# Optimization experiments

Hardware: AMD Instinct MI355X
Metric: run time of the kernel (lower is better)

## Reference

```python
import jax, jax.numpy as jnp
import numpy as np

G, B, K, D = 16384, 4, 2, 64
NEG = -1e30


def _mlp3(x, w1, b1, w2, b2, w3, b3):
    # MLP: linear->relu x3 (BatchNorm defined but unused in original forward)
    h = jax.nn.relu(x @ w1 + b1)
    h = jax.nn.relu(h @ w2 + b2)
    return jax.nn.relu(h @ w3 + b3)


def setup_inputs() -> dict:
    key = jax.random.key(0)
    ks = jax.random.split(key, 32)

    def lin(k, fan_in, fan_out):
        k1, k2 = jax.random.split(k)
        s = 1.0 / np.sqrt(fan_in)
        w = jax.random.uniform(k1, (fan_in, fan_out), jnp.float32, -s, s)
        b = jax.random.uniform(k2, (fan_out,), jnp.float32, -s, s)
        return w, b

    inp = {}
    inp['ap_feat'] = jax.random.normal(ks[0], (G, B, 1), jnp.float32)
    inp['e_feat'] = jax.random.normal(ks[1], (G, B, K, 2), jnp.float32)
    inp['w_pre_ap'], inp['b_pre_ap'] = lin(ks[2], 1, D)
    inp['w_pre_edge'], inp['b_pre_edge'] = lin(ks[3], 2, D)
    # mlp_update_5 (AP-side neighbor messages), _6 (UE-side), _7 (edge update)
    inp['w5_1'], inp['b5_1'] = lin(ks[4], 2 * D, D)
    inp['w5_2'], inp['b5_2'] = lin(ks[5], D, D)
    inp['w5_3'], inp['b5_3'] = lin(ks[6], D, D)
    inp['w6_1'], inp['b6_1'] = lin(ks[7], 2 * D, D)
    inp['w6_2'], inp['b6_2'] = lin(ks[8], D, D)
    inp['w6_3'], inp['b6_3'] = lin(ks[9], D, D)
    inp['w7_1'], inp['b7_1'] = lin(ks[10], 2 * D, D)
    inp['w7_2'], inp['b7_2'] = lin(ks[11], D, D)
    inp['w7_3'], inp['b7_3'] = lin(ks[12], D, D)
    inp['w_post'], inp['b_post'] = lin(ks[13], D, 2)
    return inp


def _edge_conv(e, a, w5_1, b5_1, w5_2, b5_2, w5_3, b5_3,
               w6_1, b6_1, w6_2, b6_2, w6_3, b6_3,
               w7_1, b7_1, w7_2, b7_2, w7_3, b7_3):
    # e: [G,B,K,D] AP2UE edge hid; a: [G,B,D] AP hid.
    # M1[g,b,j] = mlp5(cat(a[g,b], e[g,b,j])) -- same-AP neighbor edges
    x1 = jnp.concatenate([jnp.broadcast_to(a[:, :, None, :], e.shape), e], axis=-1)  # [G,B,K,2D]
    M1 = _mlp3(x1, w5_1, b5_1, w5_2, b5_2, w5_3, b5_3)  # [G,B,K,D]
    # M2[g,b,bp,k] = mlp6(cat(a[g,b], e[g,bp,k])) -- same-UE neighbor edges
    # (original uses the SRC AP feature here too). Split first linear to
    # avoid materializing the [G,B,B,K,2D] concat.
    h = jax.nn.relu(
        (a @ w6_1[:D])[:, :, None, None, :]
        + (e @ w6_1[D:])[:, None, :, :, :]
        + b6_1)  # [G,B,B,K,D]
    h = jax.nn.relu(h @ w6_2 + b6_2)
    M2 = jax.nn.relu(h @ w6_3 + b6_3)  # [G,B,Bp,K,D]
    # masked max excluding the edge itself
    eyeK = jnp.eye(K, dtype=bool)  # [k, j]
    m1max = jnp.max(jnp.where(eyeK[None, None, :, :, None], NEG,
                              M1[:, :, None, :, :]), axis=3)  # [G,B,K,D]
    eyeB = jnp.eye(B, dtype=bool)  # [b, bp]
    m2max = jnp.max(jnp.where(eyeB[None, :, :, None, None], NEG, M2), axis=2)  # [G,B,K,D]
    agg = jnp.maximum(m1max, m2max)
    # new edge feature: mlp7(cat(agg, e_hid))
    return _mlp3(jnp.concatenate([agg, e], axis=-1),
                 w7_1, b7_1, w7_2, b7_2, w7_3, b7_3)


def reference(ap_feat, e_feat, w_pre_ap, b_pre_ap, w_pre_edge, b_pre_edge,
              w5_1, b5_1, w5_2, b5_2, w5_3, b5_3,
              w6_1, b6_1, w6_2, b6_2, w6_3, b6_3,
              w7_1, b7_1, w7_2, b7_2, w7_3, b7_3,
              w_post, b_post):
    # PreLayer (live branches only: AP nodes and AP2UE edges; APConv/UEConv
    # write node 'new' which is never read, so UE/UE2AP branches are dead).
    a = jax.nn.relu(ap_feat @ w_pre_ap + b_pre_ap)   # [G,B,D]
    e = jax.nn.relu(e_feat @ w_pre_edge + b_pre_edge)  # [G,B,K,D]
    # two UpdateLayers (shared weights: ModuleList([UpdateLayer()]*2) + global MLPs)
    for _ in range(2):
        e = _edge_conv(e, a, w5_1, b5_1, w5_2, b5_2, w5_3, b5_3,
                       w6_1, b6_1, w6_2, b6_2, w6_3, b6_3,
                       w7_1, b7_1, w7_2, b7_2, w7_3, b7_3)
    out = e @ w_post + b_post  # [G,B,K,2]
    r, im = out[..., 0], out[..., 1]
    # norm_func: per-graph [B,K] complex matrix, each row (over K) L2-normalized
    n = jnp.sqrt(jnp.sum(r * r + im * im, axis=-1, keepdims=True))
    return jnp.stack([r / n, im / n], axis=-1)  # [G,B,K,2]
```

## Files before the change

### kernel.cpp

```cpp
#include <hip/hip_runtime.h>


typedef unsigned short u16;
typedef unsigned int   u32;
typedef __attribute__((ext_vector_type(8))) short short8_t;
typedef __attribute__((ext_vector_type(2))) short short2v;
typedef __attribute__((ext_vector_type(4))) float floatx4;

#define OFF_W51 0
#define OFF_W61 8192
#define OFF_W71 16384
#define OFF_W52 24576
#define OFF_W53 28672
#define OFF_W62 32768
#define OFF_W63 36864
#define OFF_W72 40960
#define OFF_W73 45056
#define WS_U16  49152

#define CB51 0
#define CB52 64
#define CB53 128
#define CB61 192
#define CB62 256
#define CB63 320
#define CB71 384
#define CB72 448
#define CB73 512
#define CWPO 576
#define CBPO 704
#define CWPA 768
#define CBPA 832
#define CWPE 896
#define CBPE 1024
#define CSZ  1088

#define PW_U16 1536

struct Params {
  const float *ap, *ef;
  const float *wpa, *bpa, *wpe, *bpe;
  const float *w51, *b51, *w52, *b52, *w53, *b53;
  const float *w61, *b61, *w62, *b62, *w63, *b63;
  const float *w71, *b71, *w72, *b72, *w73, *b73;
  const float *wpost, *bpost;
  float *out;
  int gtot;
};

__device__ __forceinline__ u32 pk2(float a, float b) {
  const u32 ua = __float_as_uint(a) + 0x8000u;
  const u32 ub = __float_as_uint(b) + 0x8000u;
  return __builtin_amdgcn_perm(ub, ua, 0x07060302u);
}
__device__ __forceinline__ float blo(u32 v) { return __uint_as_float(v << 16); }
__device__ __forceinline__ float bhi(u32 v) { return __uint_as_float(v & 0xffff0000u); }
__device__ __forceinline__ u32 pkmax(u32 a, u32 b) {
  const short2v r = __builtin_elementwise_max(__builtin_bit_cast(short2v, a),
                                              __builtin_bit_cast(short2v, b));
  return __builtin_bit_cast(u32, r);
}
__device__ __forceinline__ u32 ror16(u32 x) { return (x >> 16) | (x << 16); }
__device__ __forceinline__ float sel4(int i, float x0, float x1, float x2, float x3) {
  const float lo = (i & 1) ? x1 : x0;
  const float hi = (i & 1) ? x3 : x2;
  return (i & 2) ? hi : lo;
}

__device__ __forceinline__ floatx4 mfma16(short8_t a, short8_t b, floatx4 c) {
  return __builtin_amdgcn_mfma_f32_16x16x32_bf16(a, b, c, 0, 0, 0);
}
__device__ __forceinline__ short8_t ldA(const u16* buf, int l) {
  return *(const short8_t*)(buf + l * 8);
}

template<int TSTRIDE>
__device__ __forceinline__ void layerK64R(floatx4* acc, short8_t a0, short8_t a1,
                                          const u16* B, int l) {
#pragma unroll
  for (int t = 0; t < 4; ++t) {
    const short8_t b0 = *(const short8_t*)(B + (t * TSTRIDE + 0) * 512 + l * 8);
    const short8_t b1 = *(const short8_t*)(B + (t * TSTRIDE + 1) * 512 + l * 8);
    acc[t] = mfma16(a0, b0, acc[t]);
    acc[t] = mfma16(a1, b1, acc[t]);
  }
}

__device__ __forceinline__ void layerK128R(floatx4* acc, short8_t a0, short8_t a1,
                                           short8_t a2, short8_t a3,
                                           const u16* B, int l) {
  short8_t a[4] = {a0, a1, a2, a3};
#pragma unroll
  for (int t = 0; t < 4; ++t)
#pragma unroll
    for (int h = 0; h < 4; ++h)
      acc[t] = mfma16(a[h], *(const short8_t*)(B + (t * 4 + h) * 512 + l * 8), acc[t]);
}

__device__ __forceinline__ void scatter_relu_bf16(u16* dst, const floatx4* acc, int q, int n) {
#pragma unroll
  for (int t = 0; t < 4; ++t) {
    const int kk = (t & 1) * 2 + (n >> 3);
    u16* base = dst + (t >> 1) * 512 + (n & 7);
    const u32 v01 = pk2(fmaxf(acc[t][0], 0.f), fmaxf(acc[t][1], 0.f));
    const u32 v23 = pk2(fmaxf(acc[t][2], 0.f), fmaxf(acc[t][3], 0.f));
    base[(4 * q + 0 + 16 * kk) * 8] = (u16)v01;
    base[(4 * q + 1 + 16 * kk) * 8] = (u16)(v01 >> 16);
    base[(4 * q + 2 + 16 * kk) * 8] = (u16)v23;
    base[(4 * q + 3 + 16 * kk) * 8] = (u16)(v23 >> 16);
  }
}

__device__ __forceinline__ void scatter_bf16(u16* dst, const floatx4* acc, int q, int n) {
#pragma unroll
  for (int t = 0; t < 4; ++t) {
    const int kk = (t & 1) * 2 + (n >> 3);
    u16* base = dst + (t >> 1) * 512 + (n & 7);
    const u32 v01 = pk2(acc[t][0], acc[t][1]);
    const u32 v23 = pk2(acc[t][2], acc[t][3]);
    base[(4 * q + 0 + 16 * kk) * 8] = (u16)v01;
    base[(4 * q + 1 + 16 * kk) * 8] = (u16)(v01 >> 16);
    base[(4 * q + 2 + 16 * kk) * 8] = (u16)v23;
    base[(4 * q + 3 + 16 * kk) * 8] = (u16)(v23 >> 16);
  }
}

__device__ __forceinline__ void scatter_pk(u16* dst, const u32* src, int q, int n) {
#pragma unroll
  for (int t = 0; t < 4; ++t) {
    const int kk = (t & 1) * 2 + (n >> 3);
    u16* base = dst + (t >> 1) * 512 + (n & 7);
#pragma unroll
    for (int half = 0; half < 2; ++half) {
      const u32 v = src[2 * t + half];
      base[(4 * q + 2 * half + 0 + 16 * kk) * 8] = (u16)v;
      base[(4 * q + 2 * half + 1 + 16 * kk) * 8] = (u16)(v >> 16);
    }
  }
}

__device__ __forceinline__ void scatter_aP(u16* dst, const floatx4* acc, int q, int n,
                                           const float* cb61) {
#pragma unroll
  for (int t = 0; t < 4; ++t) {
    const int kk = (t & 1) * 2 + (n >> 3);
    u16* base = dst + (t >> 1) * 256 + (n & 7);
    const float bv = cb61[16 * t + n];
    const u32 v = pk2(acc[t][0] + bv, acc[t][2] + bv);
    base[(2 * q + 0 + 8 * kk) * 8] = (u16)v;
    base[(2 * q + 1 + 8 * kk) * 8] = (u16)(v >> 16);
  }
}

__device__ __forceinline__ void init_accL(floatx4* acc, const float* cb, int n) {
#pragma unroll
  for (int t = 0; t < 4; ++t) {
    const float b = cb[16 * t + n];
    floatx4 v; v[0] = b; v[1] = b; v[2] = b; v[3] = b;
    acc[t] = v;
  }
}

struct frag2 { short8_t f0, f1; };

__device__ __forceinline__ frag2 make_a(float apv, int q, const float* sc) {
  frag2 r;
#pragma unroll
  for (int h = 0; h < 2; ++h) {
    const int fb = 32 * h + 8 * q;
    const float4 wa0 = *(const float4*)(sc + CWPA + fb);
    const float4 wa1 = *(const float4*)(sc + CWPA + fb + 4);
    const float4 ba0 = *(const float4*)(sc + CBPA + fb);
    const float4 ba1 = *(const float4*)(sc + CBPA + fb + 4);
    uint4 pa;
    pa.x = pk2(fmaxf(fmaf(apv, wa0.x, ba0.x), 0.f), fmaxf(fmaf(apv, wa0.y, ba0.y), 0.f));
    pa.y = pk2(fmaxf(fmaf(apv, wa0.z, ba0.z), 0.f), fmaxf(fmaf(apv, wa0.w, ba0.w), 0.f));
    pa.z = pk2(fmaxf(fmaf(apv, wa1.x, ba1.x), 0.f), fmaxf(fmaf(apv, wa1.y, ba1.y), 0.f));
    pa.w = pk2(fmaxf(fmaf(apv, wa1.z, ba1.z), 0.f), fmaxf(fmaf(apv, wa1.w, ba1.w), 0.f));
    if (h == 0) r.f0 = __builtin_bit_cast(short8_t, pa);
    else        r.f1 = __builtin_bit_cast(short8_t, pa);
  }
  return r;
}

#define NBLK 256
#define NWAVE 16
#define PPW  2

__global__ __attribute__((amdgpu_waves_per_eu(4, 4), amdgpu_num_vgpr(128)))
__launch_bounds__(1024, 4)
void hetgnn_mfma(Params p) {
  __shared__ __align__(16) u16   sW[WS_U16];
  __shared__ __align__(16) u16   sAct[NWAVE * PW_U16];
  __shared__ __align__(16) float sConst[CSZ];

  const int tid  = threadIdx.x;
  const int wave = tid >> 6;
  const int l    = tid & 63;
  const int q    = l >> 4;
  const int n    = l & 15;

  {
    const float* mats[9] = {p.w51, p.w61, p.w71, p.w52, p.w53, p.w62, p.w63, p.w72, p.w73};
    for (int fi = wave; fi < 96; fi += NWAVE) {
      const float* W;
      int t, h;
      if (fi < 48) { W = mats[fi >> 4]; const int loc = fi & 15; t = loc >> 2; h = loc & 3; }
      else { const int j = fi - 48; W = mats[3 + (j >> 3)]; const int loc = j & 7; t = loc >> 1; h = loc & 1; }
      const int nn = 16 * t + n;
      const int k0 = 32 * h + q * 8;
      float w[8];
#pragma unroll
      for (int j = 0; j < 8; ++j) w[j] = W[(k0 + j) * 64 + nn];
      uint4 o;
      o.x = pk2(w[0], w[1]); o.y = pk2(w[2], w[3]);
      o.z = pk2(w[4], w[5]); o.w = pk2(w[6], w[7]);
      *(uint4*)(sW + fi * 512 + l * 8) = o;
    }
  }
  if (tid < 64) {
    sConst[CB51 + tid] = p.b51[tid];
    sConst[CB52 + tid] = p.b52[tid];
    sConst[CB53 + tid] = p.b53[tid];
    sConst[CB61 + tid] = p.b61[tid];
    sConst[CB62 + tid] = p.b62[tid];
    sConst[CB63 + tid] = p.b63[tid];
    sConst[CB71 + tid] = p.b71[tid];
    sConst[CB72 + tid] = p.b72[tid];
    sConst[CB73 + tid] = p.b73[tid];
    sConst[CWPA + tid] = p.wpa[tid];
    sConst[CBPA + tid] = p.bpa[tid];
    sConst[CBPE + tid] = p.bpe[tid];
  }
  if (tid < 128) {
    sConst[CWPO + tid] = p.wpost[tid];
    sConst[CWPE + tid] = p.wpe[tid];
  }
  if (tid < 2) sConst[CBPO + tid] = p.bpost[tid];
  __syncthreads();

  u16* BUF = sAct + wave * PW_U16;
  u16* aPb = BUF + 1024;

  const int wslot = blockIdx.x * NWAVE + wave;

  for (int pi = 0; pi < PPW; ++pi) {
    const int g0 = (wslot * PPW + pi) * 2;
    if (g0 + 2 > p.gtot) break;

    const float apv = p.ap[(g0 + (n >> 3)) * 4 + ((n >> 1) & 3)];
    const frag2 A = make_a(apv, q, sConst);
    short8_t e0, e1;
    {
      const float f0 = p.ef[(g0 + (n >> 3)) * 16 + (n & 7) * 2];
      const float f1 = p.ef[(g0 + (n >> 3)) * 16 + (n & 7) * 2 + 1];
#pragma unroll
      for (int h = 0; h < 2; ++h) {
        const int fb = 32 * h + 8 * q;
        const float4 w00 = *(const float4*)(sConst + CWPE + fb);
        const float4 w01 = *(const float4*)(sConst + CWPE + fb + 4);
        const float4 w10 = *(const float4*)(sConst + CWPE + 64 + fb);
        const float4 w11 = *(const float4*)(sConst + CWPE + 64 + fb + 4);
        const float4 be0 = *(const float4*)(sConst + CBPE + fb);
        const float4 be1 = *(const float4*)(sConst + CBPE + fb + 4);
        uint4 pe;
        pe.x = pk2(fmaxf(fmaf(f0, w00.x, fmaf(f1, w10.x, be0.x)), 0.f),
                   fmaxf(fmaf(f0, w00.y, fmaf(f1, w10.y, be0.y)), 0.f));
        pe.y = pk2(fmaxf(fmaf(f0, w00.z, fmaf(f1, w10.z, be0.z)), 0.f),
                   fmaxf(fmaf(f0, w00.w, fmaf(f1, w10.w, be0.w)), 0.f));
        pe.z = pk2(fmaxf(fmaf(f0, w01.x, fmaf(f1, w11.x, be1.x)), 0.f),
                   fmaxf(fmaf(f0, w01.y, fmaf(f1, w11.y, be1.y)), 0.f));
        pe.w = pk2(fmaxf(fmaf(f0, w01.z, fmaf(f1, w11.z, be1.z)), 0.f),
                   fmaxf(fmaf(f0, w01.w, fmaf(f1, w11.w, be1.w)), 0.f));
        if (h == 0) e0 = __builtin_bit_cast(short8_t, pe);
        else        e1 = __builtin_bit_cast(short8_t, pe);
      }
    }

    {
      floatx4 accA[4];
#pragma unroll
      for (int t = 0; t < 4; ++t) { accA[t][0] = 0.f; accA[t][1] = 0.f; accA[t][2] = 0.f; accA[t][3] = 0.f; }
      layerK64R<4>(accA, A.f0, A.f1, sW + OFF_W61, l);
      scatter_aP(aPb, accA, q, n, sConst + CB61);
    }

#pragma unroll 1
    for (int it = 0; it < 2; ++it) {
      if (it == 1) { e0 = ldA(BUF, l); e1 = ldA(BUF + 512, l); }

      u32 m1p[8];
      {
        floatx4 acc[4]; init_accL(acc, sConst + CB51, n);
        layerK128R(acc, A.f0, A.f1, e0, e1, sW + OFF_W51, l);
        scatter_relu_bf16(BUF, acc, q, n);
        floatx4 acc2[4]; init_accL(acc2, sConst + CB52, n);
        layerK64R<2>(acc2, ldA(BUF, l), ldA(BUF + 512, l), sW + OFF_W52, l);
        scatter_relu_bf16(BUF, acc2, q, n);
        floatx4 acc3[4]; init_accL(acc3, sConst + CB53, n);
        layerK64R<2>(acc3, ldA(BUF, l), ldA(BUF + 512, l), sW + OFF_W53, l);
#pragma unroll
        for (int t = 0; t < 4; ++t) {
          m1p[2 * t + 0] = pk2(acc3[t][0], acc3[t][1]);
          m1p[2 * t + 1] = pk2(acc3[t][2], acc3[t][3]);
        }
      }

      u32 m2p[8];
      {
        floatx4 accE[4];
#pragma unroll
        for (int t = 0; t < 4; ++t) { accE[t][0] = 0.f; accE[t][1] = 0.f; accE[t][2] = 0.f; accE[t][3] = 0.f; }
        layerK64R<4>(accE, e0, e1, sW + OFF_W61 + 2 * 512, l);
        scatter_bf16(BUF, accE, q, n);

        const int d = n >> 1;
        const int b_ln = d & 3;
        short8_t hf0[3], hf1[3];
#pragma unroll
        for (int j = 0; j < 3; ++j) {
          const int bp = (j >= b_ln) ? (j + 1) : j;
          const int re = (n & 8) + bp * 2 + (n & 1);
#pragma unroll
          for (int h = 0; h < 2; ++h) {
            const uint4 av = *(const uint4*)(aPb + h * 256 + (d + 8 * q) * 8);
            const uint4 ev = *(const uint4*)(BUF + h * 512 + (re + 16 * q) * 8);
            uint4 ph;
            ph.x = pk2(fmaxf(blo(av.x) + blo(ev.x), 0.f),
                       fmaxf(bhi(av.x) + bhi(ev.x), 0.f));
            ph.y = pk2(fmaxf(blo(av.y) + blo(ev.y), 0.f),
                       fmaxf(bhi(av.y) + bhi(ev.y), 0.f));
            ph.z = pk2(fmaxf(blo(av.z) + blo(ev.z), 0.f),
                       fmaxf(bhi(av.z) + bhi(ev.z), 0.f));
            ph.w = pk2(fmaxf(blo(av.w) + blo(ev.w), 0.f),
                       fmaxf(bhi(av.w) + bhi(ev.w), 0.f));
            if (h == 0) hf0[j] = __builtin_bit_cast(short8_t, ph);
            else        hf1[j] = __builtin_bit_cast(short8_t, ph);
          }
        }
#pragma unroll
        for (int j = 0; j < 3; ++j) {
          floatx4 acc2[4]; init_accL(acc2, sConst + CB62, n);
          layerK64R<2>(acc2, hf0[j], hf1[j], sW + OFF_W62, l);
          scatter_relu_bf16(BUF, acc2, q, n);
          floatx4 acc3[4]; init_accL(acc3, sConst + CB63, n);
          layerK64R<2>(acc3, ldA(BUF, l), ldA(BUF + 512, l), sW + OFF_W63, l);
#pragma unroll
          for (int t = 0; t < 4; ++t) {
#pragma unroll
            for (int h = 0; h < 2; ++h) {
              const u32 cand = pk2(acc3[t][2 * h], acc3[t][2 * h + 1]);
              m2p[2 * t + h] = (j == 0) ? cand : pkmax(m2p[2 * t + h], cand);
            }
          }
        }
      }

      {
        u32 agp[8];
#pragma unroll
        for (int i = 0; i < 8; ++i)
          agp[i] = pkmax(pkmax(ror16(m1p[i]), m2p[i]), 0u);
        scatter_pk(BUF, agp, q, n);
        floatx4 acc[4]; init_accL(acc, sConst + CB71, n);
        layerK128R(acc, ldA(BUF, l), ldA(BUF + 512, l), e0, e1, sW + OFF_W71, l);
        scatter_relu_bf16(BUF, acc, q, n);
        floatx4 acc2[4]; init_accL(acc2, sConst + CB72, n);
        layerK64R<2>(acc2, ldA(BUF, l), ldA(BUF + 512, l), sW + OFF_W72, l);
        scatter_relu_bf16(BUF, acc2, q, n);
        floatx4 acc3[4]; init_accL(acc3, sConst + CB73, n);
        layerK64R<2>(acc3, ldA(BUF, l), ldA(BUF + 512, l), sW + OFF_W73, l);

        if (it == 0) {
          scatter_relu_bf16(BUF, acc3, q, n);
        } else {
          float prr[4] = {0.f, 0.f, 0.f, 0.f}, pii[4] = {0.f, 0.f, 0.f, 0.f};
#pragma unroll
          for (int t = 0; t < 4; ++t) {
            const float wr = sConst[CWPO + (16 * t + n) * 2];
            const float wi = sConst[CWPO + (16 * t + n) * 2 + 1];
#pragma unroll
            for (int r = 0; r < 4; ++r) {
              const float e = fmaxf(acc3[t][r], 0.f);
              prr[r] = fmaf(e, wr, prr[r]);
              pii[r] = fmaf(e, wi, pii[r]);
            }
          }
          const float bpR = sConst[CBPO], bpI = sConst[CBPO + 1];
#pragma unroll
          for (int r = 0; r < 4; ++r) {
#pragma unroll
            for (int off = 1; off < 16; off <<= 1) {
              prr[r] += __shfl_xor(prr[r], off, 16);
              pii[r] += __shfl_xor(pii[r], off, 16);
            }
            prr[r] += bpR;
            pii[r] += bpI;
          }
          const int r = n >> 1, c = n & 1, rp = r ^ 1;
          const float pr_r  = sel4(r,  prr[0], prr[1], prr[2], prr[3]);
          const float pi_r  = sel4(r,  pii[0], pii[1], pii[2], pii[3]);
          const float pr_rp = sel4(rp, prr[0], prr[1], prr[2], prr[3]);
          const float pi_rp = sel4(rp, pii[0], pii[1], pii[2], pii[3]);
          const float num = c ? pi_r : pr_r;
          const float n2  = pr_r * pr_r + pi_r * pi_r + pr_rp * pr_rp + pi_rp * pi_rp;
          if (n < 8) p.out[g0 * 16 + (4 * q + r) * 2 + c] = num / sqrtf(n2);
        }
      }
    }
  }
}

extern "C" void kernel_launch(void* const* d_in, const int* in_sizes, int n_in,
                              void* d_out, int out_size, void* d_ws, size_t ws_size,
                              hipStream_t stream) {
  Params p;
  p.ap    = (const float*)d_in[0];
  p.ef    = (const float*)d_in[1];
  p.wpa   = (const float*)d_in[2];  p.bpa   = (const float*)d_in[3];
  p.wpe   = (const float*)d_in[4];  p.bpe   = (const float*)d_in[5];
  p.w51   = (const float*)d_in[6];  p.b51   = (const float*)d_in[7];
  p.w52   = (const float*)d_in[8];  p.b52   = (const float*)d_in[9];
  p.w53   = (const float*)d_in[10]; p.b53   = (const float*)d_in[11];
  p.w61   = (const float*)d_in[12]; p.b61   = (const float*)d_in[13];
  p.w62   = (const float*)d_in[14]; p.b62   = (const float*)d_in[15];
  p.w63   = (const float*)d_in[16]; p.b63   = (const float*)d_in[17];
  p.w71   = (const float*)d_in[18]; p.b71   = (const float*)d_in[19];
  p.w72   = (const float*)d_in[20]; p.b72   = (const float*)d_in[21];
  p.w73   = (const float*)d_in[22]; p.b73   = (const float*)d_in[23];
  p.wpost = (const float*)d_in[24]; p.bpost = (const float*)d_in[25];
  p.out   = (float*)d_out;
  p.gtot  = in_sizes[0] / 4;

  hipLaunchKernelGGL(hetgnn_mfma, dim3(NBLK), dim3(1024), 0, stream, p);
}
```

Baseline: 159.8 us.

## Keep MLP activations in registers via transposed MFMA, dropping LDS scatter buffers

Swaps the MFMA operand roles so weights become the A operand and activations the B operand. Each layer's output accumulator can then be packed straight into the next layer's input fragment in registers, which removes the per-wave LDS activation buffer and the scalar scatter/reload between layers. Weight and bias staging is permuted to match, neighbour gathering uses ds_bpermute and ds_swizzle, and the W62 fragments are cached in registers. The launch changes to 512 threads with 8 waves handling 4 pairs each, trading occupancy for higher register pressure.

```diff
diff --git a/kernel.cpp b/kernel.cpp
--- a/kernel.cpp
+++ b/kernel.cpp
@@ -35,8 +35,6 @@
 #define CBPE 1024
 #define CSZ  1088
 
-#define PW_U16 1536
-
 struct Params {
   const float *ap, *ef;
   const float *wpa, *bpa, *wpe, *bpe;
@@ -60,158 +58,117 @@
                                               __builtin_bit_cast(short2v, b));
   return __builtin_bit_cast(u32, r);
 }
-__device__ __forceinline__ u32 ror16(u32 x) { return (x >> 16) | (x << 16); }
-__device__ __forceinline__ float sel4(int i, float x0, float x1, float x2, float x3) {
-  const float lo = (i & 1) ? x1 : x0;
-  const float hi = (i & 1) ? x3 : x2;
-  return (i & 2) ? hi : lo;
+__device__ __forceinline__ u32 swz1(u32 x) {
+  return (u32)__builtin_amdgcn_ds_swizzle((int)x, 0x041F);
 }
 
 __device__ __forceinline__ floatx4 mfma16(short8_t a, short8_t b, floatx4 c) {
   return __builtin_amdgcn_mfma_f32_16x16x32_bf16(a, b, c, 0, 0, 0);
 }
-__device__ __forceinline__ short8_t ldA(const u16* buf, int l) {
-  return *(const short8_t*)(buf + l * 8);
-}
-
-template<int TSTRIDE>
-__device__ __forceinline__ void layerK64R(floatx4* acc, short8_t a0, short8_t a1,
-                                          const u16* B, int l) {
-#pragma unroll
-  for (int t = 0; t < 4; ++t) {
-    const short8_t b0 = *(const short8_t*)(B + (t * TSTRIDE + 0) * 512 + l * 8);
-    const short8_t b1 = *(const short8_t*)(B + (t * TSTRIDE + 1) * 512 + l * 8);
-    acc[t] = mfma16(a0, b0, acc[t]);
-    acc[t] = mfma16(a1, b1, acc[t]);
-  }
-}
-
-__device__ __forceinline__ void layerK128R(floatx4* acc, short8_t a0, short8_t a1,
-                                           short8_t a2, short8_t a3,
-                                           const u16* B, int l) {
-  short8_t a[4] = {a0, a1, a2, a3};
-#pragma unroll
-  for (int t = 0; t < 4; ++t)
-#pragma unroll
-    for (int h = 0; h < 4; ++h)
-      acc[t] = mfma16(a[h], *(const short8_t*)(B + (t * 4 + h) * 512 + l * 8), acc[t]);
-}
-
-__device__ __forceinline__ void scatter_relu_bf16(u16* dst, const floatx4* acc, int q, int n) {
-#pragma unroll
-  for (int t = 0; t < 4; ++t) {
-    const int kk = (t & 1) * 2 + (n >> 3);
-    u16* base = dst + (t >> 1) * 512 + (n & 7);
-    const u32 v01 = pk2(fmaxf(acc[t][0], 0.f), fmaxf(acc[t][1], 0.f));
-    const u32 v23 = pk2(fmaxf(acc[t][2], 0.f), fmaxf(acc[t][3], 0.f));
-    base[(4 * q + 0 + 16 * kk) * 8] = (u16)v01;
-    base[(4 * q + 1 + 16 * kk) * 8] = (u16)(v01 >> 16);
-    base[(4 * q + 2 + 16 * kk) * 8] = (u16)v23;
-    base[(4 * q + 3 + 16 * kk) * 8] = (u16)(v23 >> 16);
-  }
-}
-
-__device__ __forceinline__ void scatter_bf16(u16* dst, const floatx4* acc, int q, int n) {
-#pragma unroll
-  for (int t = 0; t < 4; ++t) {
-    const int kk = (t & 1) * 2 + (n >> 3);
-    u16* base = dst + (t >> 1) * 512 + (n & 7);
-    const u32 v01 = pk2(acc[t][0], acc[t][1]);
-    const u32 v23 = pk2(acc[t][2], acc[t][3]);
-    base[(4 * q + 0 + 16 * kk) * 8] = (u16)v01;
-    base[(4 * q + 1 + 16 * kk) * 8] = (u16)(v01 >> 16);
-    base[(4 * q + 2 + 16 * kk) * 8] = (u16)v23;
-    base[(4 * q + 3 + 16 * kk) * 8] = (u16)(v23 >> 16);
-  }
-}
-
-__device__ __forceinline__ void scatter_pk(u16* dst, const u32* src, int q, int n) {
-#pragma unroll
-  for (int t = 0; t < 4; ++t) {
-    const int kk = (t & 1) * 2 + (n >> 3);
-    u16* base = dst + (t >> 1) * 512 + (n & 7);
-#pragma unroll
-    for (int half = 0; half < 2; ++half) {
-      const u32 v = src[2 * t + half];
-      base[(4 * q + 2 * half + 0 + 16 * kk) * 8] = (u16)v;
-      base[(4 * q + 2 * half + 1 + 16 * kk) * 8] = (u16)(v >> 16);
-    }
-  }
-}
-
-__device__ __forceinline__ void scatter_aP(u16* dst, const floatx4* acc, int q, int n,
-                                           const float* cb61) {
-#pragma unroll
-  for (int t = 0; t < 4; ++t) {
-    const int kk = (t & 1) * 2 + (n >> 3);
-    u16* base = dst + (t >> 1) * 256 + (n & 7);
-    const float bv = cb61[16 * t + n];
-    const u32 v = pk2(acc[t][0] + bv, acc[t][2] + bv);
-    base[(2 * q + 0 + 8 * kk) * 8] = (u16)v;
-    base[(2 * q + 1 + 8 * kk) * 8] = (u16)(v >> 16);
-  }
-}
-
-__device__ __forceinline__ void init_accL(floatx4* acc, const float* cb, int n) {
-#pragma unroll
-  for (int t = 0; t < 4; ++t) {
-    const float b = cb[16 * t + n];
-    floatx4 v; v[0] = b; v[1] = b; v[2] = b; v[3] = b;
-    acc[t] = v;
-  }
-}
-
-struct frag2 { short8_t f0, f1; };
-
-__device__ __forceinline__ frag2 make_a(float apv, int q, const float* sc) {
-  frag2 r;
-#pragma unroll
-  for (int h = 0; h < 2; ++h) {
-    const int fb = 32 * h + 8 * q;
-    const float4 wa0 = *(const float4*)(sc + CWPA + fb);
-    const float4 wa1 = *(const float4*)(sc + CWPA + fb + 4);
-    const float4 ba0 = *(const float4*)(sc + CBPA + fb);
-    const float4 ba1 = *(const float4*)(sc + CBPA + fb + 4);
-    uint4 pa;
-    pa.x = pk2(fmaxf(fmaf(apv, wa0.x, ba0.x), 0.f), fmaxf(fmaf(apv, wa0.y, ba0.y), 0.f));
-    pa.y = pk2(fmaxf(fmaf(apv, wa0.z, ba0.z), 0.f), fmaxf(fmaf(apv, wa0.w, ba0.w), 0.f));
-    pa.z = pk2(fmaxf(fmaf(apv, wa1.x, ba1.x), 0.f), fmaxf(fmaf(apv, wa1.y, ba1.y), 0.f));
-    pa.w = pk2(fmaxf(fmaf(apv, wa1.z, ba1.z), 0.f), fmaxf(fmaf(apv, wa1.w, ba1.w), 0.f));
-    if (h == 0) r.f0 = __builtin_bit_cast(short8_t, pa);
-    else        r.f1 = __builtin_bit_cast(short8_t, pa);
-  }
-  return r;
+__device__ __forceinline__ short8_t ldW(const u16* B, int f, int l) {
+  return *(const short8_t*)(B + f * 512 + l * 8);
+}
+__device__ __forceinline__ short8_t mkf(u32 a, u32 b, u32 c, u32 d) {
+  uint4 v; v.x = a; v.y = b; v.z = c; v.w = d;
+  return __builtin_bit_cast(short8_t, v);
+}
+
+__device__ __forceinline__ void init0(floatx4* acc) {
+#pragma unroll
+  for (int t = 0; t < 4; ++t) { acc[t][0] = 0.f; acc[t][1] = 0.f; acc[t][2] = 0.f; acc[t][3] = 0.f; }
+}
+__device__ __forceinline__ void initB(floatx4* acc, const float* cb, int qp) {
+#pragma unroll
+  for (int t = 0; t < 4; ++t) {
+    const float4 b = *(const float4*)(cb + 16 * t + 4 * qp);
+    acc[t][0] = b.x; acc[t][1] = b.y; acc[t][2] = b.z; acc[t][3] = b.w;
+  }
+}
+
+template<int TS>
+__device__ __forceinline__ void layerT(floatx4* acc, const u16* W,
+                                       short8_t b0, short8_t b1, int l) {
+#pragma unroll
+  for (int t = 0; t < 4; ++t) {
+    acc[t] = mfma16(ldW(W, t * TS + 0, l), b0, acc[t]);
+    acc[t] = mfma16(ldW(W, t * TS + 1, l), b1, acc[t]);
+  }
+}
+__device__ __forceinline__ void layerT128(floatx4* acc, const u16* W,
+                                          short8_t f0, short8_t f1,
+                                          short8_t f2, short8_t f3, int l) {
+#pragma unroll
+  for (int t = 0; t < 4; ++t) {
+    acc[t] = mfma16(ldW(W, t * 4 + 0, l), f0, acc[t]);
+    acc[t] = mfma16(ldW(W, t * 4 + 1, l), f1, acc[t]);
+    acc[t] = mfma16(ldW(W, t * 4 + 2, l), f2, acc[t]);
+    acc[t] = mfma16(ldW(W, t * 4 + 3, l), f3, acc[t]);
+  }
+}
+__device__ __forceinline__ void layerB(floatx4* acc, const short8_t* Wc,
+                                       short8_t b0, short8_t b1) {
+#pragma unroll
+  for (int t = 0; t < 4; ++t) {
+    acc[t] = mfma16(Wc[2 * t + 0], b0, acc[t]);
+    acc[t] = mfma16(Wc[2 * t + 1], b1, acc[t]);
+  }
+}
+
+__device__ __forceinline__ void packRf(short8_t& f0, short8_t& f1, const floatx4* a) {
+  uint4 u0, u1;
+  u0.x = pk2(fmaxf(a[0][0], 0.f), fmaxf(a[0][1], 0.f));
+  u1.x = pk2(fmaxf(a[0][2], 0.f), fmaxf(a[0][3], 0.f));
+  u0.y = pk2(fmaxf(a[1][0], 0.f), fmaxf(a[1][1], 0.f));
+  u1.y = pk2(fmaxf(a[1][2], 0.f), fmaxf(a[1][3], 0.f));
+  u0.z = pk2(fmaxf(a[2][0], 0.f), fmaxf(a[2][1], 0.f));
+  u1.z = pk2(fmaxf(a[2][2], 0.f), fmaxf(a[2][3], 0.f));
+  u0.w = pk2(fmaxf(a[3][0], 0.f), fmaxf(a[3][1], 0.f));
+  u1.w = pk2(fmaxf(a[3][2], 0.f), fmaxf(a[3][3], 0.f));
+  f0 = __builtin_bit_cast(short8_t, u0);
+  f1 = __builtin_bit_cast(short8_t, u1);
+}
+__device__ __forceinline__ void pack0(u32* d, const floatx4* a) {
+#pragma unroll
+  for (int t = 0; t < 4; ++t) {
+    d[2 * t + 0] = pk2(a[t][0], a[t][1]);
+    d[2 * t + 1] = pk2(a[t][2], a[t][3]);
+  }
 }
 
 #define NBLK 256
-#define NWAVE 16
-#define PPW  2
-
-__global__ __attribute__((amdgpu_waves_per_eu(4, 4), amdgpu_num_vgpr(128)))
-__launch_bounds__(1024, 4)
+#define NWAVE 8
+#define PPW  4
+
+__global__ __launch_bounds__(512, 2)
+__attribute__((amdgpu_waves_per_eu(2, 2)))
 void hetgnn_mfma(Params p) {
   __shared__ __align__(16) u16   sW[WS_U16];
-  __shared__ __align__(16) u16   sAct[NWAVE * PW_U16];
   __shared__ __align__(16) float sConst[CSZ];
 
   const int tid  = threadIdx.x;
   const int wave = tid >> 6;
   const int l    = tid & 63;
-  const int q    = l >> 4;
-  const int n    = l & 15;
+  const int qp   = l >> 4;
+  const int c    = l & 15;
 
   {
-    const float* mats[9] = {p.w51, p.w61, p.w71, p.w52, p.w53, p.w62, p.w63, p.w72, p.w73};
     for (int fi = wave; fi < 96; fi += NWAVE) {
-      const float* W;
-      int t, h;
-      if (fi < 48) { W = mats[fi >> 4]; const int loc = fi & 15; t = loc >> 2; h = loc & 3; }
-      else { const int j = fi - 48; W = mats[3 + (j >> 3)]; const int loc = j & 7; t = loc >> 1; h = loc & 1; }
-      const int nn = 16 * t + n;
-      const int k0 = 32 * h + q * 8;
+      int t, h, mi;
+      if (fi < 48) { mi = fi >> 4; const int loc = fi & 15; t = loc >> 2; h = loc & 3; }
+      else { const int j2 = fi - 48; mi = 3 + (j2 >> 3); const int loc = j2 & 7; t = loc >> 1; h = loc & 1; }
+      const float* W =
+          (mi == 0) ? p.w51 : (mi == 1) ? p.w61 : (mi == 2) ? p.w71 :
+          (mi == 3) ? p.w52 : (mi == 4) ? p.w53 : (mi == 5) ? p.w62 :
+          (mi == 6) ? p.w63 : (mi == 7) ? p.w72 : p.w73;
+      const int nn = 16 * t + c;
       float w[8];
 #pragma unroll
-      for (int j = 0; j < 8; ++j) w[j] = W[(k0 + j) * 64 + nn];
+      for (int jj = 0; jj < 8; ++jj) {
+        const int kidx = (fi < 48)
+            ? 64 * (h >> 1) + 16 * (jj >> 1) + 4 * qp + 2 * (h & 1) + (jj & 1)
+            : 16 * (jj >> 1) + 4 * qp + 2 * h + (jj & 1);
+        w[jj] = W[kidx * 64 + nn];
+      }
       uint4 o;
       o.x = pk2(w[0], w[1]); o.y = pk2(w[2], w[3]);
       o.z = pk2(w[4], w[5]); o.w = pk2(w[6], w[7]);
@@ -228,183 +185,189 @@
     sConst[CB71 + tid] = p.b71[tid];
     sConst[CB72 + tid] = p.b72[tid];
     sConst[CB73 + tid] = p.b73[tid];
-    sConst[CWPA + tid] = p.wpa[tid];
-    sConst[CBPA + tid] = p.bpa[tid];
-    sConst[CBPE + tid] = p.bpe[tid];
+    sConst[CWPO + tid]      = p.wpost[2 * tid];
+    sConst[CWPO + 64 + tid] = p.wpost[2 * tid + 1];
+    {
+      const int f = tid >> 5, pp = (tid >> 3) & 3, jj = tid & 7;
+      const int feat = 16 * (jj >> 1) + 4 * pp + 2 * f + (jj & 1);
+      sConst[CWPA + tid] = p.wpa[feat];
+      sConst[CBPA + tid] = p.bpa[feat];
+      sConst[CBPE + tid] = p.bpe[feat];
+    }
   }
   if (tid < 128) {
-    sConst[CWPO + tid] = p.wpost[tid];
-    sConst[CWPE + tid] = p.wpe[tid];
+    const int s = tid & 63;
+    const int f = s >> 5, pp = (s >> 3) & 3, jj = s & 7;
+    const int feat = 16 * (jj >> 1) + 4 * pp + 2 * f + (jj & 1);
+    sConst[CWPE + tid] = p.wpe[(tid >> 6) * 64 + feat];
   }
   if (tid < 2) sConst[CBPO + tid] = p.bpost[tid];
   __syncthreads();
 
-  u16* BUF = sAct + wave * PW_U16;
-  u16* aPb = BUF + 1024;
+  short8_t w62c[8];
+#pragma unroll
+  for (int f = 0; f < 8; ++f) w62c[f] = ldW(sW + OFF_W62, f, l);
+
+  const int b_ln = (c >> 1) & 3;
+  int vnb[3];
+#pragma unroll
+  for (int j = 0; j < 3; ++j) {
+    const int bp = j + (j >= b_ln);
+    vnb[j] = ((l & 48) + (c & 8) + 2 * bp + (c & 1)) << 2;
+  }
 
   const int wslot = blockIdx.x * NWAVE + wave;
 
+#pragma unroll 1
   for (int pi = 0; pi < PPW; ++pi) {
     const int g0 = (wslot * PPW + pi) * 2;
     if (g0 + 2 > p.gtot) break;
 
-    const float apv = p.ap[(g0 + (n >> 3)) * 4 + ((n >> 1) & 3)];
-    const frag2 A = make_a(apv, q, sConst);
-    short8_t e0, e1;
+    short8_t af0, af1, ef0, ef1;
     {
-      const float f0 = p.ef[(g0 + (n >> 3)) * 16 + (n & 7) * 2];
-      const float f1 = p.ef[(g0 + (n >> 3)) * 16 + (n & 7) * 2 + 1];
-#pragma unroll
-      for (int h = 0; h < 2; ++h) {
-        const int fb = 32 * h + 8 * q;
-        const float4 w00 = *(const float4*)(sConst + CWPE + fb);
-        const float4 w01 = *(const float4*)(sConst + CWPE + fb + 4);
-        const float4 w10 = *(const float4*)(sConst + CWPE + 64 + fb);
-        const float4 w11 = *(const float4*)(sConst + CWPE + 64 + fb + 4);
-        const float4 be0 = *(const float4*)(sConst + CBPE + fb);
-        const float4 be1 = *(const float4*)(sConst + CBPE + fb + 4);
+      const float apv = p.ap[(g0 + (c >> 3)) * 4 + ((c >> 1) & 3)];
+      const float e0v = p.ef[(g0 + (c >> 3)) * 16 + (c & 7) * 2];
+      const float e1v = p.ef[(g0 + (c >> 3)) * 16 + (c & 7) * 2 + 1];
+#pragma unroll
+      for (int f = 0; f < 2; ++f) {
+        const int base = 32 * f + 8 * qp;
+        const float4 wa0 = *(const float4*)(sConst + CWPA + base);
+        const float4 wa1 = *(const float4*)(sConst + CWPA + base + 4);
+        const float4 ba0 = *(const float4*)(sConst + CBPA + base);
+        const float4 ba1 = *(const float4*)(sConst + CBPA + base + 4);
+        uint4 pa;
+        pa.x = pk2(fmaxf(fmaf(apv, wa0.x, ba0.x), 0.f), fmaxf(fmaf(apv, wa0.y, ba0.y), 0.f));
+        pa.y = pk2(fmaxf(fmaf(apv, wa0.z, ba0.z), 0.f), fmaxf(fmaf(apv, wa0.w, ba0.w), 0.f));
+        pa.z = pk2(fmaxf(fmaf(apv, wa1.x, ba1.x), 0.f), fmaxf(fmaf(apv, wa1.y, ba1.y), 0.f));
+        pa.w = pk2(fmaxf(fmaf(apv, wa1.z, ba1.z), 0.f), fmaxf(fmaf(apv, wa1.w, ba1.w), 0.f));
+        const float4 w00 = *(const float4*)(sConst + CWPE + base);
+        const float4 w01 = *(const float4*)(sConst + CWPE + base + 4);
+        const float4 w10 = *(const float4*)(sConst + CWPE + 64 + base);
+        const float4 w11 = *(const float4*)(sConst + CWPE + 64 + base + 4);
+        const float4 be0 = *(const float4*)(sConst + CBPE + base);
+        const float4 be1 = *(const float4*)(sConst + CBPE + base + 4);
         uint4 pe;
-        pe.x = pk2(fmaxf(fmaf(f0, w00.x, fmaf(f1, w10.x, be0.x)), 0.f),
-                   fmaxf(fmaf(f0, w00.y, fmaf(f1, w10.y, be0.y)), 0.f));
-        pe.y = pk2(fmaxf(fmaf(f0, w00.z, fmaf(f1, w10.z, be0.z)), 0.f),
-                   fmaxf(fmaf(f0, w00.w, fmaf(f1, w10.w, be0.w)), 0.f));
-        pe.z = pk2(fmaxf(fmaf(f0, w01.x, fmaf(f1, w11.x, be1.x)), 0.f),
-                   fmaxf(fmaf(f0, w01.y, fmaf(f1, w11.y, be1.y)), 0.f));
-        pe.w = pk2(fmaxf(fmaf(f0, w01.z, fmaf(f1, w11.z, be1.z)), 0.f),
-                   fmaxf(fmaf(f0, w01.w, fmaf(f1, w11.w, be1.w)), 0.f));
-        if (h == 0) e0 = __builtin_bit_cast(short8_t, pe);
-        else        e1 = __builtin_bit_cast(short8_t, pe);
-      }
-    }
-
+        pe.x = pk2(fmaxf(fmaf(e0v, w00.x, fmaf(e1v, w10.x, be0.x)), 0.f),
+                   fmaxf(fmaf(e0v, w00.y, fmaf(e1v, w10.y, be0.y)), 0.f));
+        pe.y = pk2(fmaxf(fmaf(e0v, w00.z, fmaf(e1v, w10.z, be0.z)), 0.f),
+                   fmaxf(fmaf(e0v, w00.w, fmaf(e1v, w10.w, be0.w)), 0.f));
+        pe.z = pk2(fmaxf(fmaf(e0v, w01.x, fmaf(e1v, w11.x, be1.x)), 0.f),
+                   fmaxf(fmaf(e0v, w01.y, fmaf(e1v, w11.y, be1.y)), 0.f));
+        pe.w = pk2(fmaxf(fmaf(e0v, w01.z, fmaf(e1v, w11.z, be1.z)), 0.f),
+                   fmaxf(fmaf(e0v, w01.w, fmaf(e1v, w11.w, be1.w)), 0.f));
+        if (f == 0) { af0 = __builtin_bit_cast(short8_t, pa); ef0 = __builtin_bit_cast(short8_t, pe); }
+        else        { af1 = __builtin_bit_cast(short8_t, pa); ef1 = __builtin_bit_cast(short8_t, pe); }
+      }
+    }
+
+    u32 aPf[8];
     {
-      floatx4 accA[4];
-#pragma unroll
-      for (int t = 0; t < 4; ++t) { accA[t][0] = 0.f; accA[t][1] = 0.f; accA[t][2] = 0.f; accA[t][3] = 0.f; }
-      layerK64R<4>(accA, A.f0, A.f1, sW + OFF_W61, l);
-      scatter_aP(aPb, accA, q, n, sConst + CB61);
+      floatx4 acc[4];
+      init0(acc);
+      layerT<4>(acc, sW + OFF_W61, af0, af1, l);
+#pragma unroll
+      for (int t = 0; t < 4; ++t) {
+        const float4 bv = *(const float4*)(sConst + CB61 + 16 * t + 4 * qp);
+        aPf[2 * t + 0] = pk2(acc[t][0] + bv.x, acc[t][1] + bv.y);
+        aPf[2 * t + 1] = pk2(acc[t][2] + bv.z, acc[t][3] + bv.w);
+      }
     }
 
 #pragma unroll 1
     for (int it = 0; it < 2; ++it) {
-      if (it == 1) { e0 = ldA(BUF, l); e1 = ldA(BUF + 512, l); }
-
       u32 m1p[8];
       {
-        floatx4 acc[4]; init_accL(acc, sConst + CB51, n);
-        layerK128R(acc, A.f0, A.f1, e0, e1, sW + OFF_W51, l);
-        scatter_relu_bf16(BUF, acc, q, n);
-        floatx4 acc2[4]; init_accL(acc2, sConst + CB52, n);
-        layerK64R<2>(acc2, ldA(BUF, l), ldA(BUF + 512, l), sW + OFF_W52, l);
-        scatter_relu_bf16(BUF, acc2, q, n);
-        floatx4 acc3[4]; init_accL(acc3, sConst + CB53, n);
-        layerK64R<2>(acc3, ldA(BUF, l), ldA(BUF + 512, l), sW + OFF_W53, l);
-#pragma unroll
-        for (int t = 0; t < 4; ++t) {
-          m1p[2 * t + 0] = pk2(acc3[t][0], acc3[t][1]);
-          m1p[2 * t + 1] = pk2(acc3[t][2], acc3[t][3]);
+        floatx4 acc[4];
+        initB(acc, sConst + CB51, qp);
+        layerT128(acc, sW + OFF_W51, af0, af1, ef0, ef1, l);
+        short8_t t0, t1;
+        packRf(t0, t1, acc);
+        initB(acc, sConst + CB52, qp);
+        layerT<2>(acc, sW + OFF_W52, t0, t1, l);
+        packRf(t0, t1, acc);
+        initB(acc, sConst + CB53, qp);
+        layerT<2>(acc, sW + OFF_W53, t0, t1, l);
+        pack0(m1p, acc);
+      }
+
+      u32 ePp[8];
+      {
+        floatx4 acc[4];
+        init0(acc);
+        layerT<4>(acc, sW + OFF_W61 + 2 * 512, ef0, ef1, l);
+        pack0(ePp, acc);
+      }
+
+      u32 m2p[8];
+#pragma unroll
+      for (int j = 0; j < 3; ++j) {
+        u32 hp[8];
+#pragma unroll
+        for (int i = 0; i < 8; ++i) {
+          const u32 ep = (u32)__builtin_amdgcn_ds_bpermute(vnb[j], (int)ePp[i]);
+          hp[i] = pk2(fmaxf(blo(aPf[i]) + blo(ep), 0.f),
+                      fmaxf(bhi(aPf[i]) + bhi(ep), 0.f));
         }
-      }
-
-      u32 m2p[8];
-      {
-        floatx4 accE[4];
-#pragma unroll
-        for (int t = 0; t < 4; ++t) { accE[t][0] = 0.f; accE[t][1] = 0.f; accE[t][2] = 0.f; accE[t][3] = 0.f; }
-        layerK64R<4>(accE, e0, e1, sW + OFF_W61 + 2 * 512, l);
-        scatter_bf16(BUF, accE, q, n);
-
-        const int d = n >> 1;
-        const int b_ln = d & 3;
-        short8_t hf0[3], hf1[3];
-#pragma unroll
-        for (int j = 0; j < 3; ++j) {
-          const int bp = (j >= b_ln) ? (j + 1) : j;
-          const int re = (n & 8) + bp * 2 + (n & 1);
-#pragma unroll
-          for (int h = 0; h < 2; ++h) {
-            const uint4 av = *(const uint4*)(aPb + h * 256 + (d + 8 * q) * 8);
-            const uint4 ev = *(const uint4*)(BUF + h * 512 + (re + 16 * q) * 8);
-            uint4 ph;
-            ph.x = pk2(fmaxf(blo(av.x) + blo(ev.x), 0.f),
-                       fmaxf(bhi(av.x) + bhi(ev.x), 0.f));
-            ph.y = pk2(fmaxf(blo(av.y) + blo(ev.y), 0.f),
-                       fmaxf(bhi(av.y) + bhi(ev.y), 0.f));
-            ph.z = pk2(fmaxf(blo(av.z) + blo(ev.z), 0.f),
-                       fmaxf(bhi(av.z) + bhi(ev.z), 0.f));
-            ph.w = pk2(fmaxf(blo(av.w) + blo(ev.w), 0.f),
-                       fmaxf(bhi(av.w) + bhi(ev.w), 0.f));
-            if (h == 0) hf0[j] = __builtin_bit_cast(short8_t, ph);
-            else        hf1[j] = __builtin_bit_cast(short8_t, ph);
-          }
-        }
-#pragma unroll
-        for (int j = 0; j < 3; ++j) {
-          floatx4 acc2[4]; init_accL(acc2, sConst + CB62, n);
-          layerK64R<2>(acc2, hf0[j], hf1[j], sW + OFF_W62, l);
-          scatter_relu_bf16(BUF, acc2, q, n);
-          floatx4 acc3[4]; init_accL(acc3, sConst + CB63, n);
-          layerK64R<2>(acc3, ldA(BUF, l), ldA(BUF + 512, l), sW + OFF_W63, l);
-#pragma unroll
-          for (int t = 0; t < 4; ++t) {
-#pragma unroll
-            for (int h = 0; h < 2; ++h) {
-              const u32 cand = pk2(acc3[t][2 * h], acc3[t][2 * h + 1]);
-              m2p[2 * t + h] = (j == 0) ? cand : pkmax(m2p[2 * t + h], cand);
-            }
-          }
-        }
+        const short8_t h0 = mkf(hp[0], hp[2], hp[4], hp[6]);
+        const short8_t h1 = mkf(hp[1], hp[3], hp[5], hp[7]);
+        floatx4 acc[4];
+        initB(acc, sConst + CB62, qp);
+        layerB(acc, w62c, h0, h1);
+        short8_t t0, t1;
+        packRf(t0, t1, acc);
+        initB(acc, sConst + CB63, qp);
+        layerT<2>(acc, sW + OFF_W63, t0, t1, l);
+        u32 cd[8];
+        pack0(cd, acc);
+#pragma unroll
+        for (int i = 0; i < 8; ++i)
+          m2p[i] = (j == 0) ? cd[i] : pkmax(m2p[i], cd[i]);
       }
 
       {
         u32 agp[8];
 #pragma unroll
         for (int i = 0; i < 8; ++i)
-          agp[i] = pkmax(pkmax(ror16(m1p[i]), m2p[i]), 0u);
-        scatter_pk(BUF, agp, q, n);
-        floatx4 acc[4]; init_accL(acc, sConst + CB71, n);
-        layerK128R(acc, ldA(BUF, l), ldA(BUF + 512, l), e0, e1, sW + OFF_W71, l);
-        scatter_relu_bf16(BUF, acc, q, n);
-        floatx4 acc2[4]; init_accL(acc2, sConst + CB72, n);
-        layerK64R<2>(acc2, ldA(BUF, l), ldA(BUF + 512, l), sW + OFF_W72, l);
-        scatter_relu_bf16(BUF, acc2, q, n);
-        floatx4 acc3[4]; init_accL(acc3, sConst + CB73, n);
-        layerK64R<2>(acc3, ldA(BUF, l), ldA(BUF + 512, l), sW + OFF_W73, l);
+          agp[i] = pkmax(pkmax(swz1(m1p[i]), m2p[i]), 0u);
+        const short8_t g0f = mkf(agp[0], agp[2], agp[4], agp[6]);
+        const short8_t g1f = mkf(agp[1], agp[3], agp[5], agp[7]);
+        floatx4 acc[4];
+        initB(acc, sConst + CB71, qp);
+        layerT128(acc, sW + OFF_W71, g0f, g1f, ef0, ef1, l);
+        short8_t t0, t1;
+        packRf(t0, t1, acc);
+        initB(acc, sConst + CB72, qp);
+        layerT<2>(acc, sW + OFF_W72, t0, t1, l);
+        packRf(t0, t1, acc);
+        initB(acc, sConst + CB73, qp);
+        layerT<2>(acc, sW + OFF_W73, t0, t1, l);
 
         if (it == 0) {
-          scatter_relu_bf16(BUF, acc3, q, n);
+          packRf(ef0, ef1, acc);
         } else {
-          float prr[4] = {0.f, 0.f, 0.f, 0.f}, pii[4] = {0.f, 0.f, 0.f, 0.f};
+          float prr = 0.f, pii = 0.f;
 #pragma unroll
           for (int t = 0; t < 4; ++t) {
-            const float wr = sConst[CWPO + (16 * t + n) * 2];
-            const float wi = sConst[CWPO + (16 * t + n) * 2 + 1];
-#pragma unroll
-            for (int r = 0; r < 4; ++r) {
-              const float e = fmaxf(acc3[t][r], 0.f);
-              prr[r] = fmaf(e, wr, prr[r]);
-              pii[r] = fmaf(e, wi, pii[r]);
-            }
+            const float4 wr = *(const float4*)(sConst + CWPO + 16 * t + 4 * qp);
+            const float4 wi = *(const float4*)(sConst + CWPO + 64 + 16 * t + 4 * qp);
+            const float e0 = fmaxf(acc[t][0], 0.f);
+            const float e1 = fmaxf(acc[t][1], 0.f);
+            const float e2 = fmaxf(acc[t][2], 0.f);
+            const float e3 = fmaxf(acc[t][3], 0.f);
+            prr = fmaf(e0, wr.x, prr); pii = fmaf(e0, wi.x, pii);
+            prr = fmaf(e1, wr.y, prr); pii = fmaf(e1, wi.y, pii);
+            prr = fmaf(e2, wr.z, prr); pii = fmaf(e2, wi.z, pii);
+            prr = fmaf(e3, wr.w, prr); pii = fmaf(e3, wi.w, pii);
           }
-          const float bpR = sConst[CBPO], bpI = sConst[CBPO + 1];
-#pragma unroll
-          for (int r = 0; r < 4; ++r) {
-#pragma unroll
-            for (int off = 1; off < 16; off <<= 1) {
-              prr[r] += __shfl_xor(prr[r], off, 16);
-              pii[r] += __shfl_xor(pii[r], off, 16);
-            }
-            prr[r] += bpR;
-            pii[r] += bpI;
-          }
-          const int r = n >> 1, c = n & 1, rp = r ^ 1;
-          const float pr_r  = sel4(r,  prr[0], prr[1], prr[2], prr[3]);
-          const float pi_r  = sel4(r,  pii[0], pii[1], pii[2], pii[3]);
-          const float pr_rp = sel4(rp, prr[0], prr[1], prr[2], prr[3]);
-          const float pi_rp = sel4(rp, pii[0], pii[1], pii[2], pii[3]);
-          const float num = c ? pi_r : pr_r;
-          const float n2  = pr_r * pr_r + pi_r * pi_r + pr_rp * pr_rp + pi_rp * pi_rp;
-          if (n < 8) p.out[g0 * 16 + (4 * q + r) * 2 + c] = num / sqrtf(n2);
+          prr += __shfl_xor(prr, 16, 64); prr += __shfl_xor(prr, 32, 64);
+          pii += __shfl_xor(pii, 16, 64); pii += __shfl_xor(pii, 32, 64);
+          prr += sConst[CBPO];
+          pii += sConst[CBPO + 1];
+          const float prn = __uint_as_float(swz1(__float_as_uint(prr)));
+          const float pin = __uint_as_float(swz1(__float_as_uint(pii)));
+          const float n2 = prr * prr + pii * pii + prn * prn + pin * pin;
+          if (qp < 2)
+            p.out[g0 * 16 + c * 2 + qp] = ((qp == 0) ? prr : pii) / sqrtf(n2);
         }
       }
     }
@@ -432,5 +395,5 @@
   p.out   = (float*)d_out;
   p.gtot  = in_sizes[0] / 4;
 
-  hipLaunchKernelGGL(hetgnn_mfma, dim3(NBLK), dim3(1024), 0, stream, p);
-}
+  hipLaunchKernelGGL(hetgnn_mfma, dim3(NBLK), dim3(512), 0, stream, p);
+}
```

Result: slower. 417.6 us (+161.4%).
